# Kernel tuning notes

Hardware: AMD Instinct MI355X
Metric: run time of the kernel (lower is better)

The kernel has to match this reference:

```python
import jax, jax.numpy as jnp
import numpy as np

N_NODES = 50000
N_EDGES = 500000
MUL0, MUL1 = 16, 8          # multiplicities of 0e and 1o irreps (in == out)
DIM = MUL0 + 3 * MUL1       # 40
N_BASIS, MID = 10, 32
WNUM = MUL0*MUL0 + MUL1*MUL0 + MUL0*MUL1 + MUL1*MUL1  # 576
INV_SQRT3 = 1.0 / np.sqrt(3.0)  # wigner-3j normalization for l=1 paths
FAN_IN = MUL0 + MUL1        # paths into each output irrep: 16 + 8 = 24
A0 = np.sqrt(1.0 / FAN_IN)  # sqrt((2*0+1)/fan_in)
A1 = np.sqrt(3.0 / FAN_IN)  # sqrt((2*1+1)/fan_in)
LN_EPS = 1e-5


def setup_inputs() -> dict:
    key = jax.random.key(0)
    ks = jax.random.split(key, 8)
    return {
        "x": jax.random.normal(ks[0], (N_NODES, DIM), jnp.float32),
        "edge_sh": jax.random.normal(ks[1], (N_EDGES, 4), jnp.float32),
        "edge_length_embedded": jax.random.uniform(ks[2], (N_EDGES, N_BASIS), jnp.float32),
        "W1": jax.random.normal(ks[3], (N_BASIS, MID), jnp.float32),
        "W2": jax.random.normal(ks[4], (MID, WNUM), jnp.float32),
        "gamma": jnp.ones((DIM,), jnp.float32),
        "beta": jnp.zeros((DIM,), jnp.float32),
        "edge_src": jax.random.randint(ks[5], (N_EDGES,), 0, N_NODES),
        "edge_dst": jax.random.randint(ks[6], (N_EDGES,), 0, N_NODES),
        "avg_num_neighbors": 10,
    }


def reference(x, edge_sh, edge_length_embedded, W1, W2, gamma, beta,
              edge_src, edge_dst, avg_num_neighbors):
    # radial MLP -> per-edge tensor-product weights (e3nn FullyConnectedNet style)
    h = jax.nn.silu(edge_length_embedded @ W1 / jnp.sqrt(jnp.float32(N_BASIS)))
    w = h @ W2 / jnp.sqrt(jnp.float32(MID))              # [E, 576]

    # gather node features onto edges and split into irrep blocks
    xg = x[edge_src]                                     # [E, 40]
    s = xg[:, :MUL0]                                     # [E, 16]  scalars 0e
    v = xg[:, MUL0:].reshape(-1, MUL1, 3)                # [E, 8, 3] vectors 1o
    sh0 = edge_sh[:, 0]                                  # [E]
    sh1 = edge_sh[:, 1:4]                                # [E, 3]

    # split per-edge weights by tensor-product path
    o0, o1, o2 = MUL0*MUL0, MUL0*MUL0 + MUL1*MUL0, MUL0*MUL0 + MUL1*MUL0 + MUL0*MUL1
    W_ss0 = w[:, :o0].reshape(-1, MUL0, MUL0)            # 0e x 0e -> 0e
    W_vv0 = w[:, o0:o1].reshape(-1, MUL1, MUL0)          # 1o x 1o -> 0e
    W_sv1 = w[:, o1:o2].reshape(-1, MUL0, MUL1)          # 0e x 1o -> 1o
    W_vs1 = w[:, o2:].reshape(-1, MUL1, MUL1)            # 1o x 0e -> 1o

    # weighted Clebsch-Gordan tensor product (per edge)
    vdot = jnp.einsum('eui,ei->eu', v, sh1) * INV_SQRT3  # CG 1x1->0
    out0 = A0 * (jnp.einsum('euk,eu->ek', W_ss0, s * sh0[:, None])
                 + jnp.einsum('euk,eu->ek', W_vv0, vdot))            # [E, 16]
    out1 = A1 * INV_SQRT3 * (
        jnp.einsum('euk,eu->ek', W_sv1, s)[:, :, None] * sh1[:, None, :]
        + jnp.einsum('euk,eui->eki', W_vs1, v) * sh0[:, None, None])  # [E, 8, 3]
    edge_values = jnp.concatenate([out0, out1.reshape(-1, 3 * MUL1)], axis=1)

    # scatter-sum into destination nodes, degree normalization, layernorm
    node = jax.ops.segment_sum(edge_values, edge_dst, num_segments=N_NODES)
    node = node / jnp.sqrt(jnp.float32(avg_num_neighbors))
    mu = node.mean(axis=-1, keepdims=True)
    var = node.var(axis=-1, keepdims=True)
    return (node - mu) * jax.lax.rsqrt(var + LN_EPS) * gamma + beta
```

## Files before the change

### kernel.cpp

```cpp
#include <hip/hip_runtime.h>
#include <hip/hip_bf16.h>

#define N_NODES 50000
#define N_EDGES 500000
#define MUL0 16
#define MUL1 8
#define DIM 40
#define N_BASIS 10
#define MID 32
#define WNUM 576
#define SCAN_BLOCKS 196
#define N_GROUPS (N_EDGES / 16)

typedef __attribute__((ext_vector_type(8))) short bf16x8_t;
typedef __attribute__((ext_vector_type(4))) float f32x4_t;

__device__ __forceinline__ float bf2f(unsigned short u) {
  return __uint_as_float(((unsigned int)u) << 16);
}
__device__ __forceinline__ unsigned short f2bf(float f) {
  unsigned int x = __float_as_uint(f);
  unsigned int r = x + 0x7fffu + ((x >> 16) & 1u);
  return (unsigned short)(r >> 16);
}
__device__ __forceinline__ bool detect_bf16(const void* gamma) {
  return ((const unsigned int*)gamma)[0] == 0x3F803F80u;
}
template <bool BF16>
__device__ __forceinline__ float ld(const void* p, size_t i) {
  if (BF16) return bf2f(((const unsigned short*)p)[i]);
  return ((const float*)p)[i];
}

#define C_INV_SQRT10 0.31622776601683794f
#define C_INV_SQRT32 0.17677669529663687f
#define C_INV_SQRT3  0.5773502691896258f
#define C_A0C        0.20412414523193154f

__device__ __forceinline__ f32x4_t mfma16x16x32(bf16x8_t a, bf16x8_t b, f32x4_t c) {
  return __builtin_amdgcn_mfma_f32_16x16x32_bf16(a, b, c, 0, 0, 0);
}

__global__ __launch_bounds__(256) void rank_kernel(
    const int* __restrict__ edge_dst, int* __restrict__ cnt,
    int* __restrict__ rank) {
  int e = blockIdx.x * 256 + threadIdx.x;
  if (e < N_EDGES) rank[e] = atomicAdd(&cnt[edge_dst[e]], 1);
}

__global__ __launch_bounds__(256) void scanA_kernel(
    const int* __restrict__ cnt, int* __restrict__ off, int* __restrict__ btot) {
  __shared__ int s[256];
  const int tid = threadIdx.x;
  const int i = blockIdx.x * 256 + tid;
  int v = (i < N_NODES) ? cnt[i] : 0;
  s[tid] = v;
  __syncthreads();
  for (int d = 1; d < 256; d <<= 1) {
    int t = (tid >= d) ? s[tid - d] : 0;
    __syncthreads();
    s[tid] += t;
    __syncthreads();
  }
  if (i < N_NODES) off[i] = s[tid] - v;
  if (tid == 255) btot[blockIdx.x] = s[255];
}

__global__ __launch_bounds__(256) void scanB_kernel(
    const int* __restrict__ btot, int* __restrict__ bbase) {
  __shared__ int s[256];
  const int tid = threadIdx.x;
  int v = (tid < SCAN_BLOCKS) ? btot[tid] : 0;
  s[tid] = v;
  __syncthreads();
  for (int d = 1; d < 256; d <<= 1) {
    int t = (tid >= d) ? s[tid - d] : 0;
    __syncthreads();
    s[tid] += t;
    __syncthreads();
  }
  if (tid < SCAN_BLOCKS) bbase[tid] = s[tid] - v;
}

__global__ __launch_bounds__(256) void scanC_kernel(
    int* __restrict__ off, const int* __restrict__ bbase) {
  const int i = blockIdx.x * 256 + threadIdx.x;
  if (i < N_NODES) off[i] += bbase[blockIdx.x];
}

__global__ __launch_bounds__(256) void posc_kernel(
    const int* __restrict__ edge_dst, const int* __restrict__ rank,
    const int* __restrict__ off, int* __restrict__ epos) {
  int e = blockIdx.x * 256 + threadIdx.x;
  if (e < N_EDGES) epos[e] = off[edge_dst[e]] + rank[e];
}


template <bool BF16>
__device__ void edge_mfma_body(
    const void* __restrict__ x,
    const void* __restrict__ edge_sh,
    const void* __restrict__ elemb,
    const void* __restrict__ W1,
    const void* __restrict__ W2,
    const int* __restrict__ edge_src,
    const int* __restrict__ epos,
    unsigned short* __restrict__ ev,
    short* __restrict__ w2b, float* __restrict__ w1s, float* __restrict__ stg)
{
  const int tid = threadIdx.x;

  for (int i = tid; i < 36 * 512; i += 256) {
    int m = i / WNUM;
    int col = i - m * WNUM;
    int q = m >> 3, j = m & 7;
    int t = col >> 4, n = col & 15;
    short val;
    if (BF16) val = (short)((const unsigned short*)W2)[i];
    else      val = (short)f2bf(((const float*)W2)[i]);
    w2b[t * 512 + q * 128 + n * 8 + j] = val;
  }
  for (int i = tid; i < N_BASIS * MID; i += 256) w1s[i] = ld<BF16>(W1, i);
  __syncthreads();

  const int lane = tid & 63;
  const int wid  = tid >> 6;
  const int quad = lane >> 4;
  const int l16  = lane & 15;
  float* S = stg + wid * 832;

  for (int gi = blockIdx.x * 4 + wid; gi < N_GROUPS; gi += gridDim.x * 4) {
    const int e0 = gi * 16;
    __builtin_amdgcn_wave_barrier();

    const int posA = epos[e0 + (lane >> 2)];
    const int posB = (lane < 16) ? epos[e0 + lane] : 0;

    if (lane < 16) {
      if (BF16) {
        uint2 sw = *reinterpret_cast<const uint2*>(
            (const unsigned short*)edge_sh + (size_t)(e0 + lane) * 4);
        S[0 * 16 + lane] = __uint_as_float(sw.x << 16);
        S[1 * 16 + lane] = __uint_as_float(sw.x & 0xffff0000u);
        S[2 * 16 + lane] = __uint_as_float(sw.y << 16);
        S[3 * 16 + lane] = __uint_as_float(sw.y & 0xffff0000u);
      } else {
        float4 s4 = *reinterpret_cast<const float4*>(
            (const float*)edge_sh + (size_t)(e0 + lane) * 4);
        S[0 * 16 + lane] = s4.x; S[1 * 16 + lane] = s4.y;
        S[2 * 16 + lane] = s4.z; S[3 * 16 + lane] = s4.w;
      }
    }

    {
      const int src = edge_src[e0 + l16];
      if (BF16) {
        const uint4* xr = reinterpret_cast<const uint4*>(
            (const unsigned short*)x + (size_t)src * DIM);
        uint4 c = xr[quad];
        unsigned wv[4] = {c.x, c.y, c.z, c.w};
        #pragma unroll
        for (int p = 0; p < 4; ++p) {
          int col = quad * 8 + 2 * p;
          float lo = __uint_as_float(wv[p] << 16);
          float hi = __uint_as_float(wv[p] & 0xffff0000u);
          int off0 = (col < 16) ? (64 + col * 16) : (448 + (col - 16) * 16);
          int off1 = (col + 1 < 16) ? (64 + (col + 1) * 16) : (448 + (col - 15) * 16);
          S[off0 + l16] = lo;
          S[off1 + l16] = hi;
        }
        if (lane < 16) {
          uint4 c4 = xr[4];
          unsigned wv4[4] = {c4.x, c4.y, c4.z, c4.w};
          #pragma unroll
          for (int p = 0; p < 4; ++p) {
            int col = 32 + 2 * p;
            S[448 + (col - 16) * 16 + lane] = __uint_as_float(wv4[p] << 16);
            S[448 + (col - 15) * 16 + lane] = __uint_as_float(wv4[p] & 0xffff0000u);
          }
        }
      } else {
        const float4* xr = reinterpret_cast<const float4*>(
            (const float*)x + (size_t)src * DIM);
        #pragma unroll
        for (int cc = 0; cc < 2; ++cc) {
          int c = quad + cc * 4;
          float4 t = xr[c];
          float vv[4] = {t.x, t.y, t.z, t.w};
          #pragma unroll
          for (int p = 0; p < 4; ++p) {
            int col = 4 * c + p;
            int offp = (col < 16) ? (64 + col * 16) : (448 + (col - 16) * 16);
            S[offp + l16] = vv[p];
          }
        }
        if (quad < 2) {
          int c = 8 + quad;
          float4 t = xr[c];
          float vv[4] = {t.x, t.y, t.z, t.w};
          #pragma unroll
          for (int p = 0; p < 4; ++p) {
            int col = 4 * c + p;
            S[448 + (col - 16) * 16 + l16] = vv[p];
          }
        }
      }
    }
    __builtin_amdgcn_wave_barrier();

    #pragma unroll
    for (int p = 0; p < 2; ++p) {
      int idx = lane + p * 64;
      int u = idx >> 4, e = idx & 15;
      float vdv = (S[448 + (u * 3 + 0) * 16 + e] * S[16 + e] +
                   S[448 + (u * 3 + 1) * 16 + e] * S[32 + e] +
                   S[448 + (u * 3 + 2) * 16 + e] * S[48 + e]) * C_INV_SQRT3;
      S[320 + u * 16 + e] = vdv;
    }
    __builtin_amdgcn_wave_barrier();

    bf16x8_t af;
    {
      float eb[N_BASIS];
      if (BF16) {
        const unsigned short* er = (const unsigned short*)elemb + (size_t)(e0 + l16) * N_BASIS;
        #pragma unroll
        for (int p = 0; p < 5; ++p) {
          unsigned uv = *reinterpret_cast<const unsigned*>(er + p * 2);
          eb[2 * p]     = __uint_as_float(uv << 16);
          eb[2 * p + 1] = __uint_as_float(uv & 0xffff0000u);
        }
      } else {
        const float* er = (const float*)elemb + (size_t)(e0 + l16) * N_BASIS;
        #pragma unroll
        for (int p = 0; p < 5; ++p) {
          float2 fv = *reinterpret_cast<const float2*>(er + p * 2);
          eb[2 * p] = fv.x; eb[2 * p + 1] = fv.y;
        }
      }
      #pragma unroll
      for (int j = 0; j < 8; ++j) {
        int k = quad * 8 + j;
        float p = 0.f;
        #pragma unroll
        for (int b = 0; b < N_BASIS; ++b) p += eb[b] * w1s[b * MID + k];
        float z = p * C_INV_SQRT10;
        float hh = z / (1.f + __expf(-z)) * C_INV_SQRT32;
        af[j] = (short)f2bf(hh);
      }
    }

    f32x4_t s0 = *reinterpret_cast<const f32x4_t*>(&S[quad * 4]);

    f32x4_t out0 = {0.f, 0.f, 0.f, 0.f};
    f32x4_t tsv  = {0.f, 0.f, 0.f, 0.f};
    f32x4_t tv0  = {0.f, 0.f, 0.f, 0.f};
    f32x4_t tv1  = {0.f, 0.f, 0.f, 0.f};
    f32x4_t tv2  = {0.f, 0.f, 0.f, 0.f};
    const f32x4_t zero = {0.f, 0.f, 0.f, 0.f};
    const int usel = (l16 >> 3);

    #pragma unroll
    for (int t = 0; t < 16; ++t) {
      bf16x8_t bf = *reinterpret_cast<const bf16x8_t*>(&w2b[t * 512 + lane * 8]);
      f32x4_t D = mfma16x16x32(af, bf, zero);
      f32x4_t sv = *reinterpret_cast<const f32x4_t*>(&S[64 + t * 16 + quad * 4]);
      out0 += D * (sv * s0);
    }
    #pragma unroll
    for (int t = 0; t < 8; ++t) {
      bf16x8_t bf = *reinterpret_cast<const bf16x8_t*>(&w2b[(16 + t) * 512 + lane * 8]);
      f32x4_t D = mfma16x16x32(af, bf, zero);
      f32x4_t vdv = *reinterpret_cast<const f32x4_t*>(&S[320 + t * 16 + quad * 4]);
      out0 += D * vdv;
    }
    #pragma unroll
    for (int t = 0; t < 8; ++t) {
      bf16x8_t bf = *reinterpret_cast<const bf16x8_t*>(&w2b[(24 + t) * 512 + lane * 8]);
      f32x4_t D = mfma16x16x32(af, bf, zero);
      int u = 2 * t + usel;
      f32x4_t sv = *reinterpret_cast<const f32x4_t*>(&S[64 + u * 16 + quad * 4]);
      tsv += D * sv;
    }
    #pragma unroll
    for (int t = 0; t < 4; ++t) {
      bf16x8_t bf = *reinterpret_cast<const bf16x8_t*>(&w2b[(32 + t) * 512 + lane * 8]);
      f32x4_t D = mfma16x16x32(af, bf, zero);
      int u = 2 * t + usel;
      f32x4_t v0 = *reinterpret_cast<const f32x4_t*>(&S[448 + (u * 3 + 0) * 16 + quad * 4]);
      f32x4_t v1 = *reinterpret_cast<const f32x4_t*>(&S[448 + (u * 3 + 1) * 16 + quad * 4]);
      f32x4_t v2 = *reinterpret_cast<const f32x4_t*>(&S[448 + (u * 3 + 2) * 16 + quad * 4]);
      tv0 += D * v0; tv1 += D * v1; tv2 += D * v2;
    }

    #pragma unroll
    for (int r = 0; r < 4; ++r) {
      tsv[r] += __shfl_xor(tsv[r], 8, 64);
      tv0[r] += __shfl_xor(tv0[r], 8, 64);
      tv1[r] += __shfl_xor(tv1[r], 8, 64);
      tv2[r] += __shfl_xor(tv2[r], 8, 64);
    }
    __builtin_amdgcn_wave_barrier();

    #pragma unroll
    for (int r = 0; r < 4; ++r)
      S[64 + (quad * 4 + r) * 42 + l16] = C_A0C * out0[r];
    if (l16 < 8) {
      f32x4_t h1x = *reinterpret_cast<const f32x4_t*>(&S[16 + quad * 4]);
      f32x4_t h1y = *reinterpret_cast<const f32x4_t*>(&S[32 + quad * 4]);
      f32x4_t h1z = *reinterpret_cast<const f32x4_t*>(&S[48 + quad * 4]);
      #pragma unroll
      for (int r = 0; r < 4; ++r) {
        int rowb = 64 + (quad * 4 + r) * 42 + 16 + 3 * l16;
        S[rowb + 0] = C_A0C * (tsv[r] * h1x[r] + tv0[r] * s0[r]);
        S[rowb + 1] = C_A0C * (tsv[r] * h1y[r] + tv1[r] * s0[r]);
        S[rowb + 2] = C_A0C * (tsv[r] * h1z[r] + tv2[r] * s0[r]);
      }
    }
    __builtin_amdgcn_wave_barrier();

    {
      const int edge = lane >> 2, chunk = lane & 3;
      const float* rp = &S[64 + edge * 42 + chunk * 8];
      unsigned p0 = (unsigned)f2bf(rp[0]) | ((unsigned)f2bf(rp[1]) << 16);
      unsigned p1 = (unsigned)f2bf(rp[2]) | ((unsigned)f2bf(rp[3]) << 16);
      unsigned p2 = (unsigned)f2bf(rp[4]) | ((unsigned)f2bf(rp[5]) << 16);
      unsigned p3 = (unsigned)f2bf(rp[6]) | ((unsigned)f2bf(rp[7]) << 16);
      uint4 t; t.x = p0; t.y = p1; t.z = p2; t.w = p3;
      *reinterpret_cast<uint4*>(ev + (size_t)posA * DIM + chunk * 8) = t;
      if (lane < 16) {
        const float* rq = &S[64 + lane * 42 + 32];
        unsigned q0 = (unsigned)f2bf(rq[0]) | ((unsigned)f2bf(rq[1]) << 16);
        unsigned q1 = (unsigned)f2bf(rq[2]) | ((unsigned)f2bf(rq[3]) << 16);
        unsigned q2 = (unsigned)f2bf(rq[4]) | ((unsigned)f2bf(rq[5]) << 16);
        unsigned q3 = (unsigned)f2bf(rq[6]) | ((unsigned)f2bf(rq[7]) << 16);
        uint4 t2; t2.x = q0; t2.y = q1; t2.z = q2; t2.w = q3;
        *reinterpret_cast<uint4*>(ev + (size_t)posB * DIM + 32) = t2;
      }
    }
  }
}

__global__ __launch_bounds__(256, 3) void edge_mfma_kernel(
    const void* __restrict__ x,
    const void* __restrict__ edge_sh,
    const void* __restrict__ elemb,
    const void* __restrict__ W1,
    const void* __restrict__ W2,
    const void* __restrict__ gamma,
    const int* __restrict__ edge_src,
    const int* __restrict__ epos,
    unsigned short* __restrict__ ev)
{
  __shared__ __align__(16) short w2b[36 * 512];
  __shared__ __align__(16) float w1s[N_BASIS * MID];
  __shared__ __align__(16) float stg[4 * 832];

  if (detect_bf16(gamma))
    edge_mfma_body<true >(x, edge_sh, elemb, W1, W2, edge_src, epos, ev, w2b, w1s, stg);
  else
    edge_mfma_body<false>(x, edge_sh, elemb, W1, W2, edge_src, epos, ev, w2b, w1s, stg);
}


template <bool BF16>
__device__ __forceinline__ void node_body(
    const unsigned short* __restrict__ ev,
    const int* __restrict__ cnt,
    const int* __restrict__ off,
    const void* __restrict__ gamma,
    const void* __restrict__ beta,
    const int* __restrict__ avg,
    void* __restrict__ out, int n)
{
  const int c = cnt[n];
  const int o = off[n];
  float s[DIM];
  #pragma unroll
  for (int d = 0; d < DIM; ++d) s[d] = 0.f;

  const uint4* p = reinterpret_cast<const uint4*>(ev + (size_t)o * DIM);
  for (int j = 0; j < c; ++j) {
    #pragma unroll
    for (int q = 0; q < 5; ++q) {
      uint4 t = p[j * 5 + q];
      unsigned int wl[4] = {t.x, t.y, t.z, t.w};
      #pragma unroll
      for (int r = 0; r < 4; ++r) {
        s[q * 8 + 2 * r]     += __uint_as_float(wl[r] << 16);
        s[q * 8 + 2 * r + 1] += __uint_as_float(wl[r] & 0xffff0000u);
      }
    }
  }

  const float inv = rsqrtf((float)avg[0]);
  float mean = 0.f;
  #pragma unroll
  for (int d = 0; d < DIM; ++d) { s[d] *= inv; mean += s[d]; }
  mean *= (1.f / DIM);
  float var = 0.f;
  #pragma unroll
  for (int d = 0; d < DIM; ++d) { float dd = s[d] - mean; var += dd * dd; }
  var *= (1.f / DIM);
  const float r = rsqrtf(var + 1e-5f);

  if (BF16) {
    #pragma unroll
    for (int d = 0; d < DIM; ++d) {
      float y = (s[d] - mean) * r * ld<true>(gamma, d) + ld<true>(beta, d);
      ((unsigned short*)out)[(size_t)n * DIM + d] = f2bf(y);
    }
  } else {
    float4* op = reinterpret_cast<float4*>((float*)out + (size_t)n * DIM);
    #pragma unroll
    for (int q = 0; q < 10; ++q) {
      float4 t;
      t.x = (s[q*4+0] - mean) * r * ld<false>(gamma, q*4+0) + ld<false>(beta, q*4+0);
      t.y = (s[q*4+1] - mean) * r * ld<false>(gamma, q*4+1) + ld<false>(beta, q*4+1);
      t.z = (s[q*4+2] - mean) * r * ld<false>(gamma, q*4+2) + ld<false>(beta, q*4+2);
      t.w = (s[q*4+3] - mean) * r * ld<false>(gamma, q*4+3) + ld<false>(beta, q*4+3);
      op[q] = t;
    }
  }
}

__global__ __launch_bounds__(256) void node_kernel(
    const unsigned short* __restrict__ ev,
    const int* __restrict__ cnt,
    const int* __restrict__ off,
    const void* __restrict__ gamma,
    const void* __restrict__ beta,
    const int* __restrict__ avg,
    void* __restrict__ out)
{
  const int n = blockIdx.x * blockDim.x + threadIdx.x;
  if (n >= N_NODES) return;
  if (detect_bf16(gamma)) node_body<true >(ev, cnt, off, gamma, beta, avg, out, n);
  else                    node_body<false>(ev, cnt, off, gamma, beta, avg, out, n);
}

extern "C" void kernel_launch(void* const* d_in, const int* in_sizes, int n_in,
                              void* d_out, int out_size, void* d_ws, size_t ws_size,
                              hipStream_t stream) {
  const void* x       = d_in[0];
  const void* edge_sh = d_in[1];
  const void* elemb   = d_in[2];
  const void* W1      = d_in[3];
  const void* W2      = d_in[4];
  const void* gamma   = d_in[5];
  const void* beta    = d_in[6];
  const int* edge_src = (const int*)d_in[7];
  const int* edge_dst = (const int*)d_in[8];
  const int* avg      = (const int*)d_in[9];

  char* wsb = (char*)d_ws;
  unsigned short* ev = (unsigned short*)(wsb);
  int* epos  = (int*)(wsb + 40000000);
  int* rank  = (int*)(wsb + 42000000);
  int* cnt   = (int*)(wsb + 44000000);
  int* off   = (int*)(wsb + 44200000);
  int* btot  = (int*)(wsb + 44400000);
  int* bbase = (int*)(wsb + 44400800);

  hipMemsetAsync(cnt, 0, 200000, stream);

  const int EB = (N_EDGES + 255) / 256;
  rank_kernel <<<EB, 256, 0, stream>>>(edge_dst, cnt, rank);
  scanA_kernel<<<SCAN_BLOCKS, 256, 0, stream>>>(cnt, off, btot);
  scanB_kernel<<<1, 256, 0, stream>>>(btot, bbase);
  scanC_kernel<<<SCAN_BLOCKS, 256, 0, stream>>>(off, bbase);
  posc_kernel <<<EB, 256, 0, stream>>>(edge_dst, rank, off, epos);

  edge_mfma_kernel<<<768, 256, 0, stream>>>(x, edge_sh, elemb, W1, W2, gamma,
                                            edge_src, epos, ev);

  node_kernel<<<SCAN_BLOCKS, 256, 0, stream>>>(ev, cnt, off,
                                               gamma, beta, avg, d_out);
}
```

Before: 224.2 us.

## Fold scan fixup into consumers, cache W2 fragments, pack bf16, split node work

Removes the scanC launch by adding the per-block scan base directly in posc and node kernels. Hoists the first 16 W2 MFMA B-fragments into registers outside the edge loop. Uses a packed two-float bf16 conversion intrinsic instead of manual rounding. Splits each node's reduction and layernorm across two threads, combining mean and variance with a lane shuffle, so more threads are in flight. The trade-off is higher register pressure in the edge kernel and extra shuffles in the node kernel.

```diff
diff --git a/kernel.cpp b/kernel.cpp
--- a/kernel.cpp
+++ b/kernel.cpp
@@ -22,6 +22,11 @@
   unsigned int x = __float_as_uint(f);
   unsigned int r = x + 0x7fffu + ((x >> 16) & 1u);
   return (unsigned short)(r >> 16);
+}
+__device__ __forceinline__ unsigned pk2bf(float a, float b) {
+  float2 f; f.x = a; f.y = b;
+  __hip_bfloat162 h = __float22bfloat162_rn(f);
+  return *reinterpret_cast<unsigned*>(&h);
 }
 __device__ __forceinline__ bool detect_bf16(const void* gamma) {
   return ((const unsigned int*)gamma)[0] == 0x3F803F80u;
@@ -82,17 +87,14 @@
   if (tid < SCAN_BLOCKS) bbase[tid] = s[tid] - v;
 }
 
-__global__ __launch_bounds__(256) void scanC_kernel(
-    int* __restrict__ off, const int* __restrict__ bbase) {
-  const int i = blockIdx.x * 256 + threadIdx.x;
-  if (i < N_NODES) off[i] += bbase[blockIdx.x];
-}
-
 __global__ __launch_bounds__(256) void posc_kernel(
     const int* __restrict__ edge_dst, const int* __restrict__ rank,
-    const int* __restrict__ off, int* __restrict__ epos) {
+    const int* __restrict__ off, const int* __restrict__ bbase,
+    int* __restrict__ epos) {
   int e = blockIdx.x * 256 + threadIdx.x;
-  if (e < N_EDGES) epos[e] = off[edge_dst[e]] + rank[e];
+  if (e >= N_EDGES) return;
+  int d = edge_dst[e];
+  epos[e] = off[d] + bbase[d >> 8] + rank[e];
 }
 
 
@@ -128,6 +130,11 @@
   const int quad = lane >> 4;
   const int l16  = lane & 15;
   float* S = stg + wid * 832;
+
+  bf16x8_t bss[16];
+  #pragma unroll
+  for (int t = 0; t < 16; ++t)
+    bss[t] = *reinterpret_cast<const bf16x8_t*>(&w2b[t * 512 + lane * 8]);
 
   for (int gi = blockIdx.x * 4 + wid; gi < N_GROUPS; gi += gridDim.x * 4) {
     const int e0 = gi * 16;
@@ -238,6 +245,7 @@
           eb[2 * p] = fv.x; eb[2 * p + 1] = fv.y;
         }
       }
+      float hv[8];
       #pragma unroll
       for (int j = 0; j < 8; ++j) {
         int k = quad * 8 + j;
@@ -245,9 +253,12 @@
         #pragma unroll
         for (int b = 0; b < N_BASIS; ++b) p += eb[b] * w1s[b * MID + k];
         float z = p * C_INV_SQRT10;
-        float hh = z / (1.f + __expf(-z)) * C_INV_SQRT32;
-        af[j] = (short)f2bf(hh);
-      }
+        hv[j] = z / (1.f + __expf(-z)) * C_INV_SQRT32;
+      }
+      __align__(16) unsigned au[4];
+      #pragma unroll
+      for (int j = 0; j < 4; ++j) au[j] = pk2bf(hv[2 * j], hv[2 * j + 1]);
+      af = *reinterpret_cast<const bf16x8_t*>(au);
     }
 
     f32x4_t s0 = *reinterpret_cast<const f32x4_t*>(&S[quad * 4]);
@@ -262,8 +273,7 @@
 
     #pragma unroll
     for (int t = 0; t < 16; ++t) {
-      bf16x8_t bf = *reinterpret_cast<const bf16x8_t*>(&w2b[t * 512 + lane * 8]);
-      f32x4_t D = mfma16x16x32(af, bf, zero);
+      f32x4_t D = mfma16x16x32(af, bss[t], zero);
       f32x4_t sv = *reinterpret_cast<const f32x4_t*>(&S[64 + t * 16 + quad * 4]);
       out0 += D * (sv * s0);
     }
@@ -322,19 +332,15 @@
     {
       const int edge = lane >> 2, chunk = lane & 3;
       const float* rp = &S[64 + edge * 42 + chunk * 8];
-      unsigned p0 = (unsigned)f2bf(rp[0]) | ((unsigned)f2bf(rp[1]) << 16);
-      unsigned p1 = (unsigned)f2bf(rp[2]) | ((unsigned)f2bf(rp[3]) << 16);
-      unsigned p2 = (unsigned)f2bf(rp[4]) | ((unsigned)f2bf(rp[5]) << 16);
-      unsigned p3 = (unsigned)f2bf(rp[6]) | ((unsigned)f2bf(rp[7]) << 16);
-      uint4 t; t.x = p0; t.y = p1; t.z = p2; t.w = p3;
+      uint4 t;
+      t.x = pk2bf(rp[0], rp[1]); t.y = pk2bf(rp[2], rp[3]);
+      t.z = pk2bf(rp[4], rp[5]); t.w = pk2bf(rp[6], rp[7]);
       *reinterpret_cast<uint4*>(ev + (size_t)posA * DIM + chunk * 8) = t;
       if (lane < 16) {
         const float* rq = &S[64 + lane * 42 + 32];
-        unsigned q0 = (unsigned)f2bf(rq[0]) | ((unsigned)f2bf(rq[1]) << 16);
-        unsigned q1 = (unsigned)f2bf(rq[2]) | ((unsigned)f2bf(rq[3]) << 16);
-        unsigned q2 = (unsigned)f2bf(rq[4]) | ((unsigned)f2bf(rq[5]) << 16);
-        unsigned q3 = (unsigned)f2bf(rq[6]) | ((unsigned)f2bf(rq[7]) << 16);
-        uint4 t2; t2.x = q0; t2.y = q1; t2.z = q2; t2.w = q3;
+        uint4 t2;
+        t2.x = pk2bf(rq[0], rq[1]); t2.y = pk2bf(rq[2], rq[3]);
+        t2.z = pk2bf(rq[4], rq[5]); t2.w = pk2bf(rq[6], rq[7]);
         *reinterpret_cast<uint4*>(ev + (size_t)posB * DIM + 32) = t2;
       }
     }
@@ -368,57 +374,57 @@
     const unsigned short* __restrict__ ev,
     const int* __restrict__ cnt,
     const int* __restrict__ off,
+    const int* __restrict__ bbase,
     const void* __restrict__ gamma,
     const void* __restrict__ beta,
     const int* __restrict__ avg,
-    void* __restrict__ out, int n)
+    void* __restrict__ out, int n, int half)
 {
   const int c = cnt[n];
-  const int o = off[n];
-  float s[DIM];
+  const int o = off[n] + bbase[n >> 8];
+  float s[20];
   #pragma unroll
-  for (int d = 0; d < DIM; ++d) s[d] = 0.f;
-
-  const uint4* p = reinterpret_cast<const uint4*>(ev + (size_t)o * DIM);
+  for (int d = 0; d < 20; ++d) s[d] = 0.f;
+
+  const uint2* p = reinterpret_cast<const uint2*>(ev) + (size_t)o * 10 + half * 5;
   for (int j = 0; j < c; ++j) {
     #pragma unroll
     for (int q = 0; q < 5; ++q) {
-      uint4 t = p[j * 5 + q];
-      unsigned int wl[4] = {t.x, t.y, t.z, t.w};
-      #pragma unroll
-      for (int r = 0; r < 4; ++r) {
-        s[q * 8 + 2 * r]     += __uint_as_float(wl[r] << 16);
-        s[q * 8 + 2 * r + 1] += __uint_as_float(wl[r] & 0xffff0000u);
-      }
+      uint2 w = p[(size_t)j * 10 + q];
+      s[q * 4 + 0] += __uint_as_float(w.x << 16);
+      s[q * 4 + 1] += __uint_as_float(w.x & 0xffff0000u);
+      s[q * 4 + 2] += __uint_as_float(w.y << 16);
+      s[q * 4 + 3] += __uint_as_float(w.y & 0xffff0000u);
     }
   }
 
   const float inv = rsqrtf((float)avg[0]);
-  float mean = 0.f;
+  float psum = 0.f;
   #pragma unroll
-  for (int d = 0; d < DIM; ++d) { s[d] *= inv; mean += s[d]; }
-  mean *= (1.f / DIM);
-  float var = 0.f;
+  for (int d = 0; d < 20; ++d) { s[d] *= inv; psum += s[d]; }
+  const float mean = (psum + __shfl_xor(psum, 1, 64)) * (1.f / DIM);
+  float pvar = 0.f;
   #pragma unroll
-  for (int d = 0; d < DIM; ++d) { float dd = s[d] - mean; var += dd * dd; }
-  var *= (1.f / DIM);
+  for (int d = 0; d < 20; ++d) { float dd = s[d] - mean; pvar += dd * dd; }
+  const float var = (pvar + __shfl_xor(pvar, 1, 64)) * (1.f / DIM);
   const float r = rsqrtf(var + 1e-5f);
 
+  const int gb = half * 20;
   if (BF16) {
     #pragma unroll
-    for (int d = 0; d < DIM; ++d) {
-      float y = (s[d] - mean) * r * ld<true>(gamma, d) + ld<true>(beta, d);
-      ((unsigned short*)out)[(size_t)n * DIM + d] = f2bf(y);
+    for (int d = 0; d < 20; ++d) {
+      float y = (s[d] - mean) * r * ld<true>(gamma, gb + d) + ld<true>(beta, gb + d);
+      ((unsigned short*)out)[(size_t)n * DIM + gb + d] = f2bf(y);
     }
   } else {
-    float4* op = reinterpret_cast<float4*>((float*)out + (size_t)n * DIM);
-    #pragma unroll
-    for (int q = 0; q < 10; ++q) {
+    float4* op = reinterpret_cast<float4*>((float*)out + (size_t)n * DIM + gb);
+    #pragma unroll
+    for (int q = 0; q < 5; ++q) {
       float4 t;
-      t.x = (s[q*4+0] - mean) * r * ld<false>(gamma, q*4+0) + ld<false>(beta, q*4+0);
-      t.y = (s[q*4+1] - mean) * r * ld<false>(gamma, q*4+1) + ld<false>(beta, q*4+1);
-      t.z = (s[q*4+2] - mean) * r * ld<false>(gamma, q*4+2) + ld<false>(beta, q*4+2);
-      t.w = (s[q*4+3] - mean) * r * ld<false>(gamma, q*4+3) + ld<false>(beta, q*4+3);
+      t.x = (s[q*4+0] - mean) * r * ld<false>(gamma, gb+q*4+0) + ld<false>(beta, gb+q*4+0);
+      t.y = (s[q*4+1] - mean) * r * ld<false>(gamma, gb+q*4+1) + ld<false>(beta, gb+q*4+1);
+      t.z = (s[q*4+2] - mean) * r * ld<false>(gamma, gb+q*4+2) + ld<false>(beta, gb+q*4+2);
+      t.w = (s[q*4+3] - mean) * r * ld<false>(gamma, gb+q*4+3) + ld<false>(beta, gb+q*4+3);
       op[q] = t;
     }
   }
@@ -428,15 +434,18 @@
     const unsigned short* __restrict__ ev,
     const int* __restrict__ cnt,
     const int* __restrict__ off,
+    const int* __restrict__ bbase,
     const void* __restrict__ gamma,
     const void* __restrict__ beta,
     const int* __restrict__ avg,
     void* __restrict__ out)
 {
-  const int n = blockIdx.x * blockDim.x + threadIdx.x;
+  const int t = blockIdx.x * blockDim.x + threadIdx.x;
+  const int n = t >> 1;
   if (n >= N_NODES) return;
-  if (detect_bf16(gamma)) node_body<true >(ev, cnt, off, gamma, beta, avg, out, n);
-  else                    node_body<false>(ev, cnt, off, gamma, beta, avg, out, n);
+  const int half = t & 1;
+  if (detect_bf16(gamma)) node_body<true >(ev, cnt, off, bbase, gamma, beta, avg, out, n, half);
+  else                    node_body<false>(ev, cnt, off, bbase, gamma, beta, avg, out, n, half);
 }
 
 extern "C" void kernel_launch(void* const* d_in, const int* in_sizes, int n_in,
@@ -468,12 +477,12 @@
   rank_kernel <<<EB, 256, 0, stream>>>(edge_dst, cnt, rank);
   scanA_kernel<<<SCAN_BLOCKS, 256, 0, stream>>>(cnt, off, btot);
   scanB_kernel<<<1, 256, 0, stream>>>(btot, bbase);
-  scanC_kernel<<<SCAN_BLOCKS, 256, 0, stream>>>(off, bbase);
-  posc_kernel <<<EB, 256, 0, stream>>>(edge_dst, rank, off, epos);
+  posc_kernel <<<EB, 256, 0, stream>>>(edge_dst, rank, off, bbase, epos);
 
   edge_mfma_kernel<<<768, 256, 0, stream>>>(x, edge_sh, elemb, W1, W2, gamma,
                                             edge_src, epos, ev);
 
-  node_kernel<<<SCAN_BLOCKS, 256, 0, stream>>>(ev, cnt, off,
-                                               gamma, beta, avg, d_out);
-}
+  const int NB2 = (2 * N_NODES + 255) / 256;
+  node_kernel<<<NB2, 256, 0, stream>>>(ev, cnt, off, bbase,
+                                       gamma, beta, avg, d_out);
+}
```

Measured after the change: 232.0 us. 3.5% more time.
